# Optimization experiments

Hardware: AMD Instinct MI355X
Metric: run time of the kernel (lower is better)

Reference implementation:

```python
import jax, jax.numpy as jnp
import numpy as np

L = 8          # n_layer
D = 512        # hidden_size
DIN = 1024     # d_inner = 2*D (Mamba expand=2)
DS = 16        # d_state
DTR = 32       # dt_rank = ceil(D/16)
K = 4          # d_conv
NACT = 3       # n_action_to_predict
ADIM = 4
LOSS_COEF = 1.0

def silu(x):
    return x * jax.nn.sigmoid(x)

def rms(x, w, eps=1e-5):
    return x * jax.lax.rsqrt(jnp.mean(x * x, axis=-1, keepdims=True) + eps) * w

def tokenize(images, states, actions, patch_w, patch_b, state_w, state_b, act_w, act_b):
    # images [b,l,3,224,224] -> 14x14 patches of 3*16*16=768 -> mean-pooled image token
    b, l = images.shape[:2]
    p = images.reshape(b, l, 3, 14, 16, 14, 16).transpose(0, 1, 3, 5, 2, 4, 6).reshape(b, l, 196, 768)
    img = jnp.mean(p @ patch_w.T + patch_b, axis=2)            # [b,l,D] token_type 1
    st = states[:, :, 0] @ state_w.T + state_b                 # [b,l,D] token_type 2
    ac = actions[:, :, :NACT - 1] @ act_w.T + act_b            # [b,l,NACT-1,D] token_type 3
    toks = jnp.concatenate([img[:, :, None], st[:, :, None], ac], axis=2)  # [b,l,1+NACT,D]
    return toks.reshape(b, l * (1 + NACT), D)

def mamba_mixer(x, in_w, cw, cb, xpw, dtw, dtb, alog, dp, ow):
    # x: [b,S,D]
    b, S, _ = x.shape
    xz = x @ in_w.T                                   # [b,S,2*DIN]
    xi, z = xz[..., :DIN], xz[..., DIN:]
    # causal depthwise conv, kernel K
    xp = jnp.pad(xi, ((0, 0), (K - 1, 0), (0, 0)))
    xc = cb + sum(cw[:, k] * xp[:, k:k + S, :] for k in range(K))
    xc = silu(xc)
    proj = xc @ xpw.T                                  # [b,S,DTR+2*DS]
    dtr, Bm, Cm = proj[..., :DTR], proj[..., DTR:DTR + DS], proj[..., DTR + DS:]
    dt = jax.nn.softplus(dtr @ dtw.T + dtb)            # [b,S,DIN]
    A = -jnp.exp(alog)                                 # [DIN,DS]
    dA = jnp.exp(dt[..., None] * A)                    # [b,S,DIN,DS]
    dBx = dt[..., None] * Bm[:, :, None, :] * xc[..., None]
    def step(h, inp):
        a_t, bx_t = inp
        h = a_t * h + bx_t
        return h, h
    _, hs = jax.lax.scan(step, jnp.zeros((b, DIN, DS), x.dtype),
                         (dA.swapaxes(0, 1), dBx.swapaxes(0, 1)))  # hs [S,b,DIN,DS]
    y = jnp.einsum('sbdn,bsn->bsd', hs, Cm) + dp * xc
    return (y * silu(z)) @ ow.T

def _forward(images, seq_length, states, actions, action_labels,
             patch_w, patch_b, state_w, state_b, act_w, act_b,
             norm1_w, in_proj_w, conv_w, conv_b, x_proj_w, dt_w, dt_b,
             A_log, Dp, out_proj_w, norm2_w, fc1_w, fc2_w, norm_f_w,
             head_w, head_b):
    b, l = images.shape[:2]
    hidden = tokenize(images, states, actions, patch_w, patch_b, state_w, state_b, act_w, act_b)
    residual = jnp.zeros_like(hidden)
    for i in range(L):
        residual = hidden + residual
        hidden = mamba_mixer(rms(residual, norm1_w[i]), in_proj_w[i], conv_w[i], conv_b[i],
                             x_proj_w[i], dt_w[i], dt_b[i], A_log[i], Dp[i], out_proj_w[i])
        residual = hidden + residual
        g = rms(residual, norm2_w[i]) @ fc1_w[i].T       # GatedMLP fc1 -> [.., 2*DIN]
        hidden = (g[..., :DIN] * silu(g[..., DIN:])) @ fc2_w[i].T
    residual = hidden + residual
    hidden = rms(residual, norm_f_w)
    # static action-token positions: per-frame tokens [img, state, act, act] -> indices 1..3
    hs = hidden.reshape(b, l, 1 + NACT, D)[:, :, 1:, :]
    action_preds = hs @ head_w.T + head_b                # [b,l,NACT,ADIM]
    mask = (jnp.arange(l)[None, :] < seq_length[:, None]).astype(jnp.float32)
    la = jnp.mean(jnp.abs(action_preds - action_labels), axis=(2, 3))
    la = (la * mask).sum(axis=1) / jnp.clip(mask.sum(axis=1), 1.0)
    loss = jnp.mean(la) * LOSS_COEF
    return loss, action_preds

def setup_inputs() -> dict:
    key = jax.random.key(0)
    ks = iter(jax.random.split(key, 40))
    nrm = lambda shape, s=0.02: s * jax.random.normal(next(ks), shape, dtype=jnp.float32)
    inp = {
        'images': jax.random.normal(next(ks), (2, 64, 3, 224, 224), jnp.float32),
        'seq_length': jax.random.randint(next(ks), (2,), 1, 65),
        'states': jax.random.normal(next(ks), (2, 64, NACT, 7), jnp.float32),
        'actions': jax.random.normal(next(ks), (2, 64, NACT, ADIM), jnp.float32),
        'action_labels': jax.random.normal(next(ks), (2, 64, NACT, ADIM), jnp.float32),
        'patch_w': nrm((D, 768)), 'patch_b': jnp.zeros((D,), jnp.float32),
        'state_w': nrm((D, 7)), 'state_b': jnp.zeros((D,), jnp.float32),
        'act_w': nrm((D, ADIM)), 'act_b': jnp.zeros((D,), jnp.float32),
        'norm1_w': jnp.ones((L, D), jnp.float32),
        'in_proj_w': nrm((L, 2 * DIN, D)),
        'conv_w': nrm((L, DIN, K), 0.1), 'conv_b': jnp.zeros((L, DIN), jnp.float32),
        'x_proj_w': nrm((L, DTR + 2 * DS, DIN)),
        'dt_w': nrm((L, DIN, DTR)), 'dt_b': jnp.full((L, DIN), -4.6, jnp.float32),
        'A_log': jnp.log(jnp.broadcast_to(jnp.arange(1, DS + 1, dtype=jnp.float32), (L, DIN, DS))).copy(),
        'Dp': jnp.ones((L, DIN), jnp.float32),
        'out_proj_w': nrm((L, D, DIN)),
        'norm2_w': jnp.ones((L, D), jnp.float32),
        'fc1_w': nrm((L, 2 * DIN, D)), 'fc2_w': nrm((L, D, DIN)),
        'norm_f_w': jnp.ones((D,), jnp.float32),
        'head_w': nrm((ADIM, D)), 'head_b': jnp.zeros((ADIM,), jnp.float32),
    }
    return inp

def reference(images, seq_length, states, actions, action_labels,
              patch_w, patch_b, state_w, state_b, act_w, act_b,
              norm1_w, in_proj_w, conv_w, conv_b, x_proj_w, dt_w, dt_b,
              A_log, Dp, out_proj_w, norm2_w, fc1_w, fc2_w, norm_f_w,
              head_w, head_b):
    return _forward(images, seq_length, states, actions, action_labels,
                    patch_w, patch_b, state_w, state_b, act_w, act_b,
                    norm1_w, in_proj_w, conv_w, conv_b, x_proj_w, dt_w, dt_b,
                    A_log, Dp, out_proj_w, norm2_w, fc1_w, fc2_w, norm_f_w,
                    head_w, head_b)
```

## Files before the change

kernel.cpp:

```cpp
#include <hip/hip_runtime.h>


#define NTOK 512
#define SEQ  256
#define CS   32
#define NC   8

typedef __attribute__((ext_vector_type(8))) short bf16x8;
typedef __attribute__((ext_vector_type(16))) float f32x16;

__device__ __forceinline__ float silu_f(float x) { return x / (1.0f + expf(-x)); }
__device__ __forceinline__ float softplus_f(float x) {
  return (x > 20.0f) ? x : log1pf(expf(x));
}

__device__ __forceinline__ void split_pack(float4 v, uint2* hi, uint2* lo) {
  uint ux = __float_as_uint(v.x), uy = __float_as_uint(v.y);
  uint uz = __float_as_uint(v.z), uw = __float_as_uint(v.w);
  hi->x = (ux >> 16) | (uy & 0xffff0000u);
  hi->y = (uz >> 16) | (uw & 0xffff0000u);
  float lx = v.x - __uint_as_float(ux & 0xffff0000u);
  float ly = v.y - __uint_as_float(uy & 0xffff0000u);
  float lz = v.z - __uint_as_float(uz & 0xffff0000u);
  float lw = v.w - __uint_as_float(uw & 0xffff0000u);
  lo->x = (__float_as_uint(lx) >> 16) | (__float_as_uint(ly) & 0xffff0000u);
  lo->y = (__float_as_uint(lz) >> 16) | (__float_as_uint(lw) & 0xffff0000u);
}

__global__ __launch_bounds__(256) void gemm_bs_k(const float* __restrict__ A,
                                                 const float* __restrict__ B,
                                                 float* __restrict__ C,
                                                 int M, int N, int K, int Kc) {
  __shared__ alignas(16) ushort sAh[2][2][2][512];
  __shared__ alignas(16) ushort sAl[2][2][2][512];
  __shared__ alignas(16) ushort sBh[2][2][2][512];
  __shared__ alignas(16) ushort sBl[2][2][2][512];
  int t = threadIdx.x;
  int bn = blockIdx.x, bm = blockIdx.y, z = blockIdx.z;
  const float* Ab = A + (size_t)bm * 64 * K + (size_t)z * Kc;
  const float* Bb = B + (size_t)bn * 64 * K + (size_t)z * Kc;
  float* Cb = C + (size_t)z * M * N;
  int r = t >> 2, kc = (t & 3) << 2;
  int st = r >> 5, m = r & 31;
  int off = ((kc >> 3) << 8) + (m << 3) + (kc & 7);
  int w = t >> 6, lane = t & 63;
  int wr = w >> 1, wc = w & 1;

  f32x16 acc;
#pragma unroll
  for (int i = 0; i < 16; ++i) acc[i] = 0.f;

  int ns = Kc >> 5;
  const float* Ar = Ab + (size_t)r * K + kc;
  const float* Br = Bb + (size_t)r * K + kc;
  float4 a0 = *(const float4*)&Ar[0];
  float4 a1 = *(const float4*)&Ar[16];
  float4 b0 = *(const float4*)&Br[0];
  float4 b1 = *(const float4*)&Br[16];
  {
    uint2 hi, lo;
    split_pack(a0, &hi, &lo);
    *(uint2*)&sAh[0][0][st][off] = hi; *(uint2*)&sAl[0][0][st][off] = lo;
    split_pack(a1, &hi, &lo);
    *(uint2*)&sAh[0][1][st][off] = hi; *(uint2*)&sAl[0][1][st][off] = lo;
    split_pack(b0, &hi, &lo);
    *(uint2*)&sBh[0][0][st][off] = hi; *(uint2*)&sBl[0][0][st][off] = lo;
    split_pack(b1, &hi, &lo);
    *(uint2*)&sBh[0][1][st][off] = hi; *(uint2*)&sBl[0][1][st][off] = lo;
  }
  __syncthreads();
  for (int ssi = 0; ssi < ns; ++ssi) {
    int buf = ssi & 1;
    if (ssi + 1 < ns) {
      a0 = *(const float4*)&Ar[(ssi + 1) * 32];
      a1 = *(const float4*)&Ar[(ssi + 1) * 32 + 16];
      b0 = *(const float4*)&Br[(ssi + 1) * 32];
      b1 = *(const float4*)&Br[(ssi + 1) * 32 + 16];
    }
    bf16x8 ah = *(bf16x8*)&sAh[buf][0][wr][lane << 3];
    bf16x8 al = *(bf16x8*)&sAl[buf][0][wr][lane << 3];
    bf16x8 bh = *(bf16x8*)&sBh[buf][0][wc][lane << 3];
    bf16x8 bl = *(bf16x8*)&sBl[buf][0][wc][lane << 3];
    acc = __builtin_amdgcn_mfma_f32_32x32x16_bf16(ah, bh, acc, 0, 0, 0);
    acc = __builtin_amdgcn_mfma_f32_32x32x16_bf16(al, bh, acc, 0, 0, 0);
    acc = __builtin_amdgcn_mfma_f32_32x32x16_bf16(ah, bl, acc, 0, 0, 0);
    bf16x8 ah1 = *(bf16x8*)&sAh[buf][1][wr][lane << 3];
    bf16x8 al1 = *(bf16x8*)&sAl[buf][1][wr][lane << 3];
    bf16x8 bh1 = *(bf16x8*)&sBh[buf][1][wc][lane << 3];
    bf16x8 bl1 = *(bf16x8*)&sBl[buf][1][wc][lane << 3];
    acc = __builtin_amdgcn_mfma_f32_32x32x16_bf16(ah1, bh1, acc, 0, 0, 0);
    acc = __builtin_amdgcn_mfma_f32_32x32x16_bf16(al1, bh1, acc, 0, 0, 0);
    acc = __builtin_amdgcn_mfma_f32_32x32x16_bf16(ah1, bl1, acc, 0, 0, 0);
    if (ssi + 1 < ns) {
      uint2 hi, lo;
      split_pack(a0, &hi, &lo);
      *(uint2*)&sAh[buf ^ 1][0][st][off] = hi; *(uint2*)&sAl[buf ^ 1][0][st][off] = lo;
      split_pack(a1, &hi, &lo);
      *(uint2*)&sAh[buf ^ 1][1][st][off] = hi; *(uint2*)&sAl[buf ^ 1][1][st][off] = lo;
      split_pack(b0, &hi, &lo);
      *(uint2*)&sBh[buf ^ 1][0][st][off] = hi; *(uint2*)&sBl[buf ^ 1][0][st][off] = lo;
      split_pack(b1, &hi, &lo);
      *(uint2*)&sBh[buf ^ 1][1][st][off] = hi; *(uint2*)&sBl[buf ^ 1][1][st][off] = lo;
    }
    __syncthreads();
  }
  int col = lane & 31, rq = lane >> 5;
  float* Cw = Cb + (size_t)(bm * 64 + wr * 32) * N + bn * 64 + wc * 32 + col;
#pragma unroll
  for (int rg = 0; rg < 16; ++rg) {
    int row = (rg & 3) + ((rg >> 2) << 3) + (rq << 2);
    Cw[(size_t)row * N] = acc[rg];
  }
}

__global__ __launch_bounds__(256) void gemm_glu_k(const float* __restrict__ G,
                                                  const float* __restrict__ B,
                                                  float* __restrict__ C,
                                                  int M, int N, int K, int Kc) {
  __shared__ alignas(16) ushort sAh[2][2][2][512];
  __shared__ alignas(16) ushort sAl[2][2][2][512];
  __shared__ alignas(16) ushort sBh[2][2][2][512];
  __shared__ alignas(16) ushort sBl[2][2][2][512];
  int t = threadIdx.x;
  int bn = blockIdx.x, bm = blockIdx.y, z = blockIdx.z;
  const float* Gb = G + (size_t)bm * 64 * 2048 + (size_t)z * Kc;
  const float* Bb = B + (size_t)bn * 64 * K + (size_t)z * Kc;
  float* Cb = C + (size_t)z * M * N;
  int r = t >> 2, kc = (t & 3) << 2;
  int st = r >> 5, m = r & 31;
  int off = ((kc >> 3) << 8) + (m << 3) + (kc & 7);
  int w = t >> 6, lane = t & 63;
  int wr = w >> 1, wc = w & 1;

  f32x16 acc;
#pragma unroll
  for (int i = 0; i < 16; ++i) acc[i] = 0.f;

  int ns = Kc >> 5;
  const float* gr = Gb + (size_t)r * 2048 + kc;
  const float* Br = Bb + (size_t)r * K + kc;
  float4 ga0 = *(const float4*)&gr[0];
  float4 gz0 = *(const float4*)&gr[1024];
  float4 ga1 = *(const float4*)&gr[16];
  float4 gz1 = *(const float4*)&gr[1040];
  float4 b0 = *(const float4*)&Br[0];
  float4 b1 = *(const float4*)&Br[16];
  {
    float4 a0 = {ga0.x * silu_f(gz0.x), ga0.y * silu_f(gz0.y),
                 ga0.z * silu_f(gz0.z), ga0.w * silu_f(gz0.w)};
    float4 a1 = {ga1.x * silu_f(gz1.x), ga1.y * silu_f(gz1.y),
                 ga1.z * silu_f(gz1.z), ga1.w * silu_f(gz1.w)};
    uint2 hi, lo;
    split_pack(a0, &hi, &lo);
    *(uint2*)&sAh[0][0][st][off] = hi; *(uint2*)&sAl[0][0][st][off] = lo;
    split_pack(a1, &hi, &lo);
    *(uint2*)&sAh[0][1][st][off] = hi; *(uint2*)&sAl[0][1][st][off] = lo;
    split_pack(b0, &hi, &lo);
    *(uint2*)&sBh[0][0][st][off] = hi; *(uint2*)&sBl[0][0][st][off] = lo;
    split_pack(b1, &hi, &lo);
    *(uint2*)&sBh[0][1][st][off] = hi; *(uint2*)&sBl[0][1][st][off] = lo;
  }
  __syncthreads();
  for (int ssi = 0; ssi < ns; ++ssi) {
    int buf = ssi & 1;
    if (ssi + 1 < ns) {
      ga0 = *(const float4*)&gr[(ssi + 1) * 32];
      gz0 = *(const float4*)&gr[1024 + (ssi + 1) * 32];
      ga1 = *(const float4*)&gr[(ssi + 1) * 32 + 16];
      gz1 = *(const float4*)&gr[1040 + (ssi + 1) * 32];
      b0 = *(const float4*)&Br[(ssi + 1) * 32];
      b1 = *(const float4*)&Br[(ssi + 1) * 32 + 16];
    }
    bf16x8 ah = *(bf16x8*)&sAh[buf][0][wr][lane << 3];
    bf16x8 al = *(bf16x8*)&sAl[buf][0][wr][lane << 3];
    bf16x8 bh = *(bf16x8*)&sBh[buf][0][wc][lane << 3];
    bf16x8 bl = *(bf16x8*)&sBl[buf][0][wc][lane << 3];
    acc = __builtin_amdgcn_mfma_f32_32x32x16_bf16(ah, bh, acc, 0, 0, 0);
    acc = __builtin_amdgcn_mfma_f32_32x32x16_bf16(al, bh, acc, 0, 0, 0);
    acc = __builtin_amdgcn_mfma_f32_32x32x16_bf16(ah, bl, acc, 0, 0, 0);
    bf16x8 ah1 = *(bf16x8*)&sAh[buf][1][wr][lane << 3];
    bf16x8 al1 = *(bf16x8*)&sAl[buf][1][wr][lane << 3];
    bf16x8 bh1 = *(bf16x8*)&sBh[buf][1][wc][lane << 3];
    bf16x8 bl1 = *(bf16x8*)&sBl[buf][1][wc][lane << 3];
    acc = __builtin_amdgcn_mfma_f32_32x32x16_bf16(ah1, bh1, acc, 0, 0, 0);
    acc = __builtin_amdgcn_mfma_f32_32x32x16_bf16(al1, bh1, acc, 0, 0, 0);
    acc = __builtin_amdgcn_mfma_f32_32x32x16_bf16(ah1, bl1, acc, 0, 0, 0);
    if (ssi + 1 < ns) {
      float4 a0 = {ga0.x * silu_f(gz0.x), ga0.y * silu_f(gz0.y),
                   ga0.z * silu_f(gz0.z), ga0.w * silu_f(gz0.w)};
      float4 a1 = {ga1.x * silu_f(gz1.x), ga1.y * silu_f(gz1.y),
                   ga1.z * silu_f(gz1.z), ga1.w * silu_f(gz1.w)};
      uint2 hi, lo;
      split_pack(a0, &hi, &lo);
      *(uint2*)&sAh[buf ^ 1][0][st][off] = hi; *(uint2*)&sAl[buf ^ 1][0][st][off] = lo;
      split_pack(a1, &hi, &lo);
      *(uint2*)&sAh[buf ^ 1][1][st][off] = hi; *(uint2*)&sAl[buf ^ 1][1][st][off] = lo;
      split_pack(b0, &hi, &lo);
      *(uint2*)&sBh[buf ^ 1][0][st][off] = hi; *(uint2*)&sBl[buf ^ 1][0][st][off] = lo;
      split_pack(b1, &hi, &lo);
      *(uint2*)&sBh[buf ^ 1][1][st][off] = hi; *(uint2*)&sBl[buf ^ 1][1][st][off] = lo;
    }
    __syncthreads();
  }
  int col = lane & 31, rq = lane >> 5;
  float* Cw = Cb + (size_t)(bm * 64 + wr * 32) * N + bn * 64 + wc * 32 + col;
#pragma unroll
  for (int rg = 0; rg < 16; ++rg) {
    int row = (rg & 3) + ((rg >> 2) << 3) + (rq << 2);
    Cw[(size_t)row * N] = acc[rg];
  }
}

__global__ void patch_part_k(const float* __restrict__ img, float* __restrict__ pmp) {
  int blk = blockIdx.x;
  int bl = blk / 14, hb = blk % 14;
  int t = threadIdx.x;
  int c = t >> 6, hi = (t >> 2) & 15, wi4 = t & 3;
  const float* base = img + (size_t)bl * 3 * 50176 + (size_t)c * 50176 +
                      (size_t)(hb * 16 + hi) * 224 + wi4 * 4;
  float4 s = {0.f, 0.f, 0.f, 0.f};
#pragma unroll
  for (int wb = 0; wb < 14; ++wb) {
    float4 v = *(const float4*)&base[wb * 16];
    s.x += v.x; s.y += v.y; s.z += v.z; s.w += v.w;
  }
  ((float4*)(pmp + (size_t)blk * 768))[t] = s;
}

__global__ void patch_red_k(const float* __restrict__ pmp, float* __restrict__ meanp) {
  int bl = blockIdx.x;
  int t = threadIdx.x;
  float4 s = {0.f, 0.f, 0.f, 0.f};
  for (int hb = 0; hb < 14; ++hb) {
    float4 v = ((const float4*)(pmp + (size_t)(bl * 14 + hb) * 768))[t];
    s.x += v.x; s.y += v.y; s.z += v.z; s.w += v.w;
  }
  const float inv = 1.0f / 196.0f;
  float4 o = {s.x * inv, s.y * inv, s.z * inv, s.w * inv};
  ((float4*)(meanp + (size_t)bl * 768))[t] = o;
}

__global__ void tokenize_k(const float* __restrict__ imgp,
                           const float* __restrict__ states,
                           const float* __restrict__ actions,
                           const float* __restrict__ pb,
                           const float* __restrict__ sw, const float* __restrict__ sb,
                           const float* __restrict__ aw, const float* __restrict__ ab,
                           float* __restrict__ hidden, float* __restrict__ residual) {
  int tok = blockIdx.x;
  int t = threadIdx.x;
  int j = tok & 3;
  int bl = tok >> 2;
  int o0 = t * 4;
  float out[4];
  if (j == 0) {
    float4 a = ((const float4*)pb)[t];
    const float* ip = imgp + (size_t)bl * 512;
#pragma unroll
    for (int p = 0; p < 8; ++p) {
      float4 v = ((const float4*)(ip + (size_t)p * 65536))[t];
      a.x += v.x; a.y += v.y; a.z += v.z; a.w += v.w;
    }
    out[0] = a.x; out[1] = a.y; out[2] = a.z; out[3] = a.w;
  } else if (j == 1) {
    const float* sv = states + (size_t)bl * 21;
#pragma unroll
    for (int i = 0; i < 4; ++i) {
      int o = o0 + i;
      float acc = sb[o];
      for (int k = 0; k < 7; ++k) acc += sw[o * 7 + k] * sv[k];
      out[i] = acc;
    }
  } else {
    const float* av = actions + ((size_t)bl * 3 + (j - 2)) * 4;
#pragma unroll
    for (int i = 0; i < 4; ++i) {
      int o = o0 + i;
      float acc = ab[o];
      for (int k = 0; k < 4; ++k) acc += aw[o * 4 + k] * av[k];
      out[i] = acc;
    }
  }
  float4 ov = {out[0], out[1], out[2], out[3]};
  ((float4*)(hidden + (size_t)tok * 512))[t] = ov;
  float4 z4 = {0.f, 0.f, 0.f, 0.f};
  ((float4*)(residual + (size_t)tok * 512))[t] = z4;
}

__global__ void addnorm_k(const float* __restrict__ hid, int parts,
                          float* __restrict__ res,
                          const float* __restrict__ w, float* __restrict__ xn) {
  int tok = blockIdx.x;
  int t = threadIdx.x;
  float4* r4 = (float4*)(res + (size_t)tok * 512);
  float4 r = r4[t];
  const float4* hp = (const float4*)(hid + (size_t)tok * 512);
  for (int p = 0; p < parts; ++p) {
    float4 h = hp[t];
    r.x += h.x; r.y += h.y; r.z += h.z; r.w += h.w;
    hp += 65536;
  }
  r4[t] = r;
  float ss = r.x * r.x + r.y * r.y + r.z * r.z + r.w * r.w;
  for (int off = 32; off; off >>= 1) ss += __shfl_down(ss, off, 64);
  __shared__ float s2[2];
  if ((t & 63) == 0) s2[t >> 6] = ss;
  __syncthreads();
  float tot = s2[0] + s2[1];
  float scale = rsqrtf(tot * (1.0f / 512.0f) + 1e-5f);
  float4 wv = ((const float4*)w)[t];
  float4 o = {r.x * scale * wv.x, r.y * scale * wv.y,
              r.z * scale * wv.z, r.w * scale * wv.w};
  ((float4*)(xn + (size_t)tok * 512))[t] = o;
}

__global__ __launch_bounds__(256) void convproj_k(const float* __restrict__ xz,
                                                  const float* __restrict__ cw,
                                                  const float* __restrict__ cb,
                                                  const float* __restrict__ xpw,
                                                  const float* __restrict__ dtw,
                                                  const float* __restrict__ dtbias,
                                                  float* __restrict__ xc,
                                                  float* __restrict__ proj,
                                                  float* __restrict__ dt) {
  int tok = blockIdx.x;
  int t = threadIdx.x;
  int b = tok >> 8, s = tok & 255;
  __shared__ float xr[1024];
  __shared__ float pp[4][64];
  __shared__ float pr[64];
  int d4 = t * 4;
  float4 cw0 = ((const float4*)cw)[d4];
  float4 cw1 = ((const float4*)cw)[d4 + 1];
  float4 cw2 = ((const float4*)cw)[d4 + 2];
  float4 cw3 = ((const float4*)cw)[d4 + 3];
  float acc0 = cb[d4], acc1 = cb[d4 + 1], acc2 = cb[d4 + 2], acc3 = cb[d4 + 3];
  const float* base = xz + (size_t)b * 256 * 2048 + d4;
  const float wk0[4] = {cw0.x, cw0.y, cw0.z, cw0.w};
  const float wk1[4] = {cw1.x, cw1.y, cw1.z, cw1.w};
  const float wk2[4] = {cw2.x, cw2.y, cw2.z, cw2.w};
  const float wk3[4] = {cw3.x, cw3.y, cw3.z, cw3.w};
#pragma unroll
  for (int k = 0; k < 4; ++k) {
    int row = s + k - 3;
    if (row >= 0) {
      float4 v = *(const float4*)&base[(size_t)row * 2048];
      acc0 += wk0[k] * v.x; acc1 += wk1[k] * v.y;
      acc2 += wk2[k] * v.z; acc3 += wk3[k] * v.w;
    }
  }
  float4 xc4 = {silu_f(acc0), silu_f(acc1), silu_f(acc2), silu_f(acc3)};
  ((float4*)(xc + (size_t)tok * 1024))[t] = xc4;
  *(float4*)&xr[d4] = xc4;
  __syncthreads();
  int n = t & 63, q = t >> 6;
  {
    const float* wrow = xpw + (size_t)n * 1024 + q * 256;
    const float* xq = xr + q * 256;
    float acc = 0.f;
    for (int k = 0; k < 256; k += 4)
      acc += wrow[k] * xq[k] + wrow[k + 1] * xq[k + 1] +
             wrow[k + 2] * xq[k + 2] + wrow[k + 3] * xq[k + 3];
    pp[q][n] = acc;
  }
  __syncthreads();
  if (t < 64) {
    float v = pp[0][t] + pp[1][t] + pp[2][t] + pp[3][t];
    pr[t] = v;
    proj[(size_t)tok * 64 + t] = v;
  }
  __syncthreads();
#pragma unroll
  for (int i = 0; i < 4; ++i) {
    int d = t * 4 + i;
    const float* dw = dtw + (size_t)d * 32;
    float a = dtbias[d];
    for (int k = 0; k < 32; ++k) a += dw[k] * pr[k];
    dt[(size_t)tok * 1024 + d] = softplus_f(a);
  }
}

__global__ __launch_bounds__(512) void scan_k(const float* __restrict__ dt,
                                              const float* __restrict__ proj,
                                              const float* __restrict__ xc,
                                              const float* __restrict__ xz,
                                              const float* __restrict__ alog,
                                              const float* __restrict__ Dp,
                                              float* __restrict__ yz) {
  __shared__ float sDt[256][4];
  __shared__ float sXc[256][4];
  __shared__ float sZ[256][4];
  __shared__ float sBC[256][32];
  __shared__ float2 sP[8][4][16];
  __shared__ float sY[256][4];
  int t = threadIdx.x;
  int g = blockIdx.x;
  int b = g >> 8;
  int d0 = (g & 255) << 2;
  int c = t >> 6, dl = (t >> 4) & 3, n = t & 15;
  int d = d0 + dl;
  const float* dtb = dt + (size_t)b * 256 * 1024 + d0;
  const float* xcb = xc + (size_t)b * 256 * 1024 + d0;
  const float* zb  = xz + (size_t)b * 256 * 2048 + 1024 + d0;
  const float* pbp = proj + (size_t)b * 256 * 64 + 32;
  float* yb = yz + (size_t)b * 256 * 1024 + d0;

  if (t < 256) {
    *(float4*)&sDt[t][0] = *(const float4*)&dtb[(size_t)t * 1024];
    *(float4*)&sZ[t][0]  = *(const float4*)&zb[(size_t)t * 2048];
  } else {
    int u = t - 256;
    *(float4*)&sXc[u][0] = *(const float4*)&xcb[(size_t)u * 1024];
  }
#pragma unroll
  for (int i = 0; i < 4; ++i) {
    int idx = i * 512 + t;
    int s = idx >> 3, c4 = (idx & 7) << 2;
    *(float4*)&sBC[s][c4] = *(const float4*)&pbp[(size_t)s * 64 + c4];
  }
  float A = -expf(alog[d * 16 + n]);
  float dp = Dp[d];
  __syncthreads();

  float Ap = 1.f, Bacc = 0.f;
#pragma unroll
  for (int i = 0; i < CS; ++i) {
    int s = (c << 5) + i;
    float dtv = sDt[s][dl];
    float dA = __expf(dtv * A);
    Bacc = dA * Bacc + dtv * sBC[s][n] * sXc[s][dl];
    Ap *= dA;
  }
  sP[c][dl][n] = make_float2(Ap, Bacc);
  __syncthreads();

  float h = 0.f;
  for (int cc = 0; cc < c; ++cc) {
    float2 p = sP[cc][dl][n];
    h = p.x * h + p.y;
  }

#pragma unroll
  for (int i = 0; i < CS; ++i) {
    int s = (c << 5) + i;
    float dtv = sDt[s][dl];
    float xcv = sXc[s][dl];
    float dA = __expf(dtv * A);
    h = dA * h + dtv * sBC[s][n] * xcv;
    float yc = h * sBC[s][16 + n];
    yc += __shfl_xor(yc, 1, 64);
    yc += __shfl_xor(yc, 2, 64);
    yc += __shfl_xor(yc, 4, 64);
    yc += __shfl_xor(yc, 8, 64);
    if (n == 0) sY[s][dl] = (yc + dp * xcv) * silu_f(sZ[s][dl]);
  }
  __syncthreads();
  if (t < 256)
    *(float4*)&yb[(size_t)t * 1024] = *(const float4*)&sY[t][0];
}

__global__ void head_k(const float* __restrict__ hf, const float* __restrict__ hw,
                       const float* __restrict__ hb, const float* __restrict__ labels,
                       float* __restrict__ preds, float* __restrict__ labs) {
  int blk = blockIdx.x;
  int j = blk % 3;
  int l = (blk / 3) % 64;
  int b = blk / 192;
  int row = b * 256 + l * 4 + 1 + j;
  int t = threadIdx.x;
  const float* x = hf + (size_t)row * 512;
  float acc[4] = {0.f, 0.f, 0.f, 0.f};
  for (int k = t; k < 512; k += 64) {
    float xv = x[k];
#pragma unroll
    for (int a = 0; a < 4; ++a) acc[a] += xv * hw[a * 512 + k];
  }
  for (int off = 32; off; off >>= 1) {
#pragma unroll
    for (int a = 0; a < 4; ++a) acc[a] += __shfl_down(acc[a], off, 64);
  }
  if (t == 0) {
    const float* lab = labels + (size_t)blk * 4;
    float sd = 0.f;
#pragma unroll
    for (int a = 0; a < 4; ++a) {
      float p = acc[a] + hb[a];
      preds[(size_t)blk * 4 + a] = p;
      sd += fabsf(p - lab[a]);
    }
    labs[blk] = sd;
  }
}

__global__ void loss_k(const float* __restrict__ labs, const int* __restrict__ seqlen,
                       float* __restrict__ out) {
  int t = threadIdx.x;
  int b = t >> 6, l = t & 63;
  float la = (labs[(b * 64 + l) * 3] + labs[(b * 64 + l) * 3 + 1] +
              labs[(b * 64 + l) * 3 + 2]) * (1.0f / 12.0f);
  float m = (l < seqlen[b]) ? 1.f : 0.f;
  float v = la * m;
  for (int off = 32; off; off >>= 1) {
    v += __shfl_down(v, off, 64);
    m += __shfl_down(m, off, 64);
  }
  __shared__ float sb_[2];
  if ((t & 63) == 0) sb_[b] = v / fmaxf(m, 1.0f);
  __syncthreads();
  if (t == 0) out[0] = 0.5f * (sb_[0] + sb_[1]);
}

extern "C" void kernel_launch(void* const* d_in, const int* in_sizes, int n_in,
                              void* d_out, int out_size, void* d_ws, size_t ws_size,
                              hipStream_t stream) {
  const float* images     = (const float*)d_in[0];
  const int*   seq_length = (const int*)d_in[1];
  const float* states     = (const float*)d_in[2];
  const float* actions    = (const float*)d_in[3];
  const float* labels     = (const float*)d_in[4];
  const float* patch_w    = (const float*)d_in[5];
  const float* patch_b    = (const float*)d_in[6];
  const float* state_w    = (const float*)d_in[7];
  const float* state_b    = (const float*)d_in[8];
  const float* act_w      = (const float*)d_in[9];
  const float* act_b      = (const float*)d_in[10];
  const float* norm1_w    = (const float*)d_in[11];
  const float* in_proj_w  = (const float*)d_in[12];
  const float* conv_w     = (const float*)d_in[13];
  const float* conv_b     = (const float*)d_in[14];
  const float* x_proj_w   = (const float*)d_in[15];
  const float* dt_w       = (const float*)d_in[16];
  const float* dt_b       = (const float*)d_in[17];
  const float* A_log      = (const float*)d_in[18];
  const float* Dp         = (const float*)d_in[19];
  const float* out_proj_w = (const float*)d_in[20];
  const float* norm2_w    = (const float*)d_in[21];
  const float* fc1_w      = (const float*)d_in[22];
  const float* fc2_w      = (const float*)d_in[23];
  const float* norm_f_w   = (const float*)d_in[24];
  const float* head_w     = (const float*)d_in[25];
  const float* head_b     = (const float*)d_in[26];

  float* out = (float*)d_out;

  float* ws = (float*)d_ws;
  float* meanp    = ws; ws += 98304;
  float* hidden   = ws; ws += 262144;
  float* residual = ws; ws += 262144;
  float* xn       = ws; ws += 262144;
  float* xz       = ws; ws += 1048576;
  float* xc       = ws; ws += 524288;
  float* proj     = ws; ws += 32768;
  float* dtbuf    = ws; ws += 524288;
  float* yz       = ws; ws += 524288;
  float* labs     = ws; ws += 384;
  float* cpart    = ws; ws += 1048576;
  float* pmp      = ws; ws += 1376256;

  hipLaunchKernelGGL(patch_part_k, dim3(1792), dim3(192), 0, stream, images, pmp);
  hipLaunchKernelGGL(patch_red_k, dim3(128), dim3(192), 0, stream, pmp, meanp);
  hipLaunchKernelGGL(gemm_bs_k, dim3(8, 2, 8), dim3(256), 0, stream,
                     meanp, patch_w, cpart, 128, 512, 768, 96);
  hipLaunchKernelGGL(tokenize_k, dim3(512), dim3(128), 0, stream, cpart, states, actions,
                     patch_b, state_w, state_b, act_w, act_b, hidden, residual);

  for (int i = 0; i < 8; ++i) {
    const float* n1 = norm1_w + i * 512;
    const float* ipw = in_proj_w + (size_t)i * 2048 * 512;
    const float* cw = conv_w + (size_t)i * 4096;
    const float* cb = conv_b + (size_t)i * 1024;
    const float* xpw = x_proj_w + (size_t)i * 65536;
    const float* dtw = dt_w + (size_t)i * 32768;
    const float* dtbias = dt_b + (size_t)i * 1024;
    const float* al = A_log + (size_t)i * 16384;
    const float* dpp = Dp + (size_t)i * 1024;
    const float* opw = out_proj_w + (size_t)i * 524288;
    const float* n2 = norm2_w + i * 512;
    const float* f1 = fc1_w + (size_t)i * 1048576;
    const float* f2 = fc2_w + (size_t)i * 524288;

    if (i == 0)
      hipLaunchKernelGGL(addnorm_k, dim3(512), dim3(128), 0, stream,
                         hidden, 1, residual, n1, xn);
    else
      hipLaunchKernelGGL(addnorm_k, dim3(512), dim3(128), 0, stream,
                         cpart, 4, residual, n1, xn);
    hipLaunchKernelGGL(gemm_bs_k, dim3(32, 8, 1), dim3(256), 0, stream,
                       xn, ipw, xz, 512, 2048, 512, 512);
    hipLaunchKernelGGL(convproj_k, dim3(512), dim3(256), 0, stream,
                       xz, cw, cb, xpw, dtw, dtbias, xc, proj, dtbuf);
    hipLaunchKernelGGL(scan_k, dim3(512), dim3(512), 0, stream,
                       dtbuf, proj, xc, xz, al, dpp, yz);
    hipLaunchKernelGGL(gemm_bs_k, dim3(8, 8, 4), dim3(256), 0, stream,
                       yz, opw, cpart, 512, 512, 1024, 256);
    hipLaunchKernelGGL(addnorm_k, dim3(512), dim3(128), 0, stream,
                       cpart, 4, residual, n2, xn);
    hipLaunchKernelGGL(gemm_bs_k, dim3(32, 8, 1), dim3(256), 0, stream,
                       xn, f1, xz, 512, 2048, 512, 512);
    hipLaunchKernelGGL(gemm_glu_k, dim3(8, 8, 4), dim3(256), 0, stream,
                       xz, f2, cpart, 512, 512, 1024, 256);
  }

  hipLaunchKernelGGL(addnorm_k, dim3(512), dim3(128), 0, stream,
                     cpart, 4, residual, norm_f_w, xn);
  hipLaunchKernelGGL(head_k, dim3(384), dim3(64), 0, stream, xn, head_w, head_b, labels,
                     out + 1, labs);
  hipLaunchKernelGGL(loss_k, dim3(1), dim3(128), 0, stream, labs, seq_length, out);
}
```

Before: 1.117 ms.

## Fuse per-layer kernels into one persistent cooperative megakernel with grid syncs

Replaces the roughly 70 separate kernel launches (GEMMs, addnorm, conv/proj, scan, tokenize, head, loss) with a single cooperative persistent kernel. Each stage loops over virtual blocks and is separated from the next by grid.sync(), with shared memory overlaid through a union-like buffer. The aim is to remove launch overhead and inter-kernel gaps. In exchange, the grid is capped by occupancy, so stages may serialize over fewer blocks, and every grid barrier has its own cost. Addnorm is adapted to 256 threads with float2.

```diff
diff --git a/kernel.cpp b/kernel.cpp
--- a/kernel.cpp
+++ b/kernel.cpp
@@ -1,10 +1,8 @@
 #include <hip/hip_runtime.h>
-
-
-#define NTOK 512
-#define SEQ  256
-#define CS   32
-#define NC   8
+#include <hip/hip_cooperative_groups.h>
+
+namespace cg = cooperative_groups;
+
 
 typedef __attribute__((ext_vector_type(8))) short bf16x8;
 typedef __attribute__((ext_vector_type(16))) float f32x16;
@@ -27,16 +25,33 @@
   lo->y = (__float_as_uint(lz) >> 16) | (__float_as_uint(lw) & 0xffff0000u);
 }
 
-__global__ __launch_bounds__(256) void gemm_bs_k(const float* __restrict__ A,
-                                                 const float* __restrict__ B,
-                                                 float* __restrict__ C,
-                                                 int M, int N, int K, int Kc) {
-  __shared__ alignas(16) ushort sAh[2][2][2][512];
-  __shared__ alignas(16) ushort sAl[2][2][2][512];
-  __shared__ alignas(16) ushort sBh[2][2][2][512];
-  __shared__ alignas(16) ushort sBl[2][2][2][512];
-  int t = threadIdx.x;
-  int bn = blockIdx.x, bm = blockIdx.y, z = blockIdx.z;
+struct GemmLds {
+  ushort sAh[2][2][2][512];
+  ushort sAl[2][2][2][512];
+  ushort sBh[2][2][2][512];
+  ushort sBl[2][2][2][512];
+};
+struct ScanLds {
+  float sDt[256][4];
+  float sXc[256][4];
+  float sZ[256][4];
+  float sBC[256][32];
+  float2 sP[8][4][16];
+  float sY[256][4];
+};
+struct ConvLds {
+  float xr[1024];
+  float pp[4][64];
+  float pr[64];
+};
+#define SMEM_BYTES 53248
+
+__device__ __forceinline__ void st_gemm(const float* __restrict__ A,
+                                        const float* __restrict__ B,
+                                        float* __restrict__ C,
+                                        int M, int N, int K, int Kc,
+                                        int bn, int bm, int z, int t, char* smem) {
+  GemmLds& L = *(GemmLds*)smem;
   const float* Ab = A + (size_t)bm * 64 * K + (size_t)z * Kc;
   const float* Bb = B + (size_t)bn * 64 * K + (size_t)z * Kc;
   float* Cb = C + (size_t)z * M * N;
@@ -60,13 +75,13 @@
   {
     uint2 hi, lo;
     split_pack(a0, &hi, &lo);
-    *(uint2*)&sAh[0][0][st][off] = hi; *(uint2*)&sAl[0][0][st][off] = lo;
+    *(uint2*)&L.sAh[0][0][st][off] = hi; *(uint2*)&L.sAl[0][0][st][off] = lo;
     split_pack(a1, &hi, &lo);
-    *(uint2*)&sAh[0][1][st][off] = hi; *(uint2*)&sAl[0][1][st][off] = lo;
+    *(uint2*)&L.sAh[0][1][st][off] = hi; *(uint2*)&L.sAl[0][1][st][off] = lo;
     split_pack(b0, &hi, &lo);
-    *(uint2*)&sBh[0][0][st][off] = hi; *(uint2*)&sBl[0][0][st][off] = lo;
+    *(uint2*)&L.sBh[0][0][st][off] = hi; *(uint2*)&L.sBl[0][0][st][off] = lo;
     split_pack(b1, &hi, &lo);
-    *(uint2*)&sBh[0][1][st][off] = hi; *(uint2*)&sBl[0][1][st][off] = lo;
+    *(uint2*)&L.sBh[0][1][st][off] = hi; *(uint2*)&L.sBl[0][1][st][off] = lo;
   }
   __syncthreads();
   for (int ssi = 0; ssi < ns; ++ssi) {
@@ -77,30 +92,30 @@
       b0 = *(const float4*)&Br[(ssi + 1) * 32];
       b1 = *(const float4*)&Br[(ssi + 1) * 32 + 16];
     }
-    bf16x8 ah = *(bf16x8*)&sAh[buf][0][wr][lane << 3];
-    bf16x8 al = *(bf16x8*)&sAl[buf][0][wr][lane << 3];
-    bf16x8 bh = *(bf16x8*)&sBh[buf][0][wc][lane << 3];
-    bf16x8 bl = *(bf16x8*)&sBl[buf][0][wc][lane << 3];
+    bf16x8 ah = *(bf16x8*)&L.sAh[buf][0][wr][lane << 3];
+    bf16x8 al = *(bf16x8*)&L.sAl[buf][0][wr][lane << 3];
+    bf16x8 bh = *(bf16x8*)&L.sBh[buf][0][wc][lane << 3];
+    bf16x8 bl = *(bf16x8*)&L.sBl[buf][0][wc][lane << 3];
     acc = __builtin_amdgcn_mfma_f32_32x32x16_bf16(ah, bh, acc, 0, 0, 0);
     acc = __builtin_amdgcn_mfma_f32_32x32x16_bf16(al, bh, acc, 0, 0, 0);
     acc = __builtin_amdgcn_mfma_f32_32x32x16_bf16(ah, bl, acc, 0, 0, 0);
-    bf16x8 ah1 = *(bf16x8*)&sAh[buf][1][wr][lane << 3];
-    bf16x8 al1 = *(bf16x8*)&sAl[buf][1][wr][lane << 3];
-    bf16x8 bh1 = *(bf16x8*)&sBh[buf][1][wc][lane << 3];
-    bf16x8 bl1 = *(bf16x8*)&sBl[buf][1][wc][lane << 3];
+    bf16x8 ah1 = *(bf16x8*)&L.sAh[buf][1][wr][lane << 3];
+    bf16x8 al1 = *(bf16x8*)&L.sAl[buf][1][wr][lane << 3];
+    bf16x8 bh1 = *(bf16x8*)&L.sBh[buf][1][wc][lane << 3];
+    bf16x8 bl1 = *(bf16x8*)&L.sBl[buf][1][wc][lane << 3];
     acc = __builtin_amdgcn_mfma_f32_32x32x16_bf16(ah1, bh1, acc, 0, 0, 0);
     acc = __builtin_amdgcn_mfma_f32_32x32x16_bf16(al1, bh1, acc, 0, 0, 0);
     acc = __builtin_amdgcn_mfma_f32_32x32x16_bf16(ah1, bl1, acc, 0, 0, 0);
     if (ssi + 1 < ns) {
       uint2 hi, lo;
       split_pack(a0, &hi, &lo);
-      *(uint2*)&sAh[buf ^ 1][0][st][off] = hi; *(uint2*)&sAl[buf ^ 1][0][st][off] = lo;
+      *(uint2*)&L.sAh[buf ^ 1][0][st][off] = hi; *(uint2*)&L.sAl[buf ^ 1][0][st][off] = lo;
       split_pack(a1, &hi, &lo);
-      *(uint2*)&sAh[buf ^ 1][1][st][off] = hi; *(uint2*)&sAl[buf ^ 1][1][st][off] = lo;
+      *(uint2*)&L.sAh[buf ^ 1][1][st][off] = hi; *(uint2*)&L.sAl[buf ^ 1][1][st][off] = lo;
       split_pack(b0, &hi, &lo);
-      *(uint2*)&sBh[buf ^ 1][0][st][off] = hi; *(uint2*)&sBl[buf ^ 1][0][st][off] = lo;
+      *(uint2*)&L.sBh[buf ^ 1][0][st][off] = hi; *(uint2*)&L.sBl[buf ^ 1][0][st][off] = lo;
       split_pack(b1, &hi, &lo);
-      *(uint2*)&sBh[buf ^ 1][1][st][off] = hi; *(uint2*)&sBl[buf ^ 1][1][st][off] = lo;
+      *(uint2*)&L.sBh[buf ^ 1][1][st][off] = hi; *(uint2*)&L.sBl[buf ^ 1][1][st][off] = lo;
     }
     __syncthreads();
   }
@@ -113,16 +128,12 @@
   }
 }
 
-__global__ __launch_bounds__(256) void gemm_glu_k(const float* __restrict__ G,
-                                                  const float* __restrict__ B,
-                                                  float* __restrict__ C,
-                                                  int M, int N, int K, int Kc) {
-  __shared__ alignas(16) ushort sAh[2][2][2][512];
-  __shared__ alignas(16) ushort sAl[2][2][2][512];
-  __shared__ alignas(16) ushort sBh[2][2][2][512];
-  __shared__ alignas(16) ushort sBl[2][2][2][512];
-  int t = threadIdx.x;
-  int bn = blockIdx.x, bm = blockIdx.y, z = blockIdx.z;
+__device__ __forceinline__ void st_glu(const float* __restrict__ G,
+                                       const float* __restrict__ B,
+                                       float* __restrict__ C,
+                                       int M, int N, int K, int Kc,
+                                       int bn, int bm, int z, int t, char* smem) {
+  GemmLds& L = *(GemmLds*)smem;
   const float* Gb = G + (size_t)bm * 64 * 2048 + (size_t)z * Kc;
   const float* Bb = B + (size_t)bn * 64 * K + (size_t)z * Kc;
   float* Cb = C + (size_t)z * M * N;
@@ -152,13 +163,13 @@
                  ga1.z * silu_f(gz1.z), ga1.w * silu_f(gz1.w)};
     uint2 hi, lo;
     split_pack(a0, &hi, &lo);
-    *(uint2*)&sAh[0][0][st][off] = hi; *(uint2*)&sAl[0][0][st][off] = lo;
+    *(uint2*)&L.sAh[0][0][st][off] = hi; *(uint2*)&L.sAl[0][0][st][off] = lo;
     split_pack(a1, &hi, &lo);
-    *(uint2*)&sAh[0][1][st][off] = hi; *(uint2*)&sAl[0][1][st][off] = lo;
+    *(uint2*)&L.sAh[0][1][st][off] = hi; *(uint2*)&L.sAl[0][1][st][off] = lo;
     split_pack(b0, &hi, &lo);
-    *(uint2*)&sBh[0][0][st][off] = hi; *(uint2*)&sBl[0][0][st][off] = lo;
+    *(uint2*)&L.sBh[0][0][st][off] = hi; *(uint2*)&L.sBl[0][0][st][off] = lo;
     split_pack(b1, &hi, &lo);
-    *(uint2*)&sBh[0][1][st][off] = hi; *(uint2*)&sBl[0][1][st][off] = lo;
+    *(uint2*)&L.sBh[0][1][st][off] = hi; *(uint2*)&L.sBl[0][1][st][off] = lo;
   }
   __syncthreads();
   for (int ssi = 0; ssi < ns; ++ssi) {
@@ -171,17 +182,17 @@
       b0 = *(const float4*)&Br[(ssi + 1) * 32];
       b1 = *(const float4*)&Br[(ssi + 1) * 32 + 16];
     }
-    bf16x8 ah = *(bf16x8*)&sAh[buf][0][wr][lane << 3];
-    bf16x8 al = *(bf16x8*)&sAl[buf][0][wr][lane << 3];
-    bf16x8 bh = *(bf16x8*)&sBh[buf][0][wc][lane << 3];
-    bf16x8 bl = *(bf16x8*)&sBl[buf][0][wc][lane << 3];
+    bf16x8 ah = *(bf16x8*)&L.sAh[buf][0][wr][lane << 3];
+    bf16x8 al = *(bf16x8*)&L.sAl[buf][0][wr][lane << 3];
+    bf16x8 bh = *(bf16x8*)&L.sBh[buf][0][wc][lane << 3];
+    bf16x8 bl = *(bf16x8*)&L.sBl[buf][0][wc][lane << 3];
     acc = __builtin_amdgcn_mfma_f32_32x32x16_bf16(ah, bh, acc, 0, 0, 0);
     acc = __builtin_amdgcn_mfma_f32_32x32x16_bf16(al, bh, acc, 0, 0, 0);
     acc = __builtin_amdgcn_mfma_f32_32x32x16_bf16(ah, bl, acc, 0, 0, 0);
-    bf16x8 ah1 = *(bf16x8*)&sAh[buf][1][wr][lane << 3];
-    bf16x8 al1 = *(bf16x8*)&sAl[buf][1][wr][lane << 3];
-    bf16x8 bh1 = *(bf16x8*)&sBh[buf][1][wc][lane << 3];
-    bf16x8 bl1 = *(bf16x8*)&sBl[buf][1][wc][lane << 3];
+    bf16x8 ah1 = *(bf16x8*)&L.sAh[buf][1][wr][lane << 3];
+    bf16x8 al1 = *(bf16x8*)&L.sAl[buf][1][wr][lane << 3];
+    bf16x8 bh1 = *(bf16x8*)&L.sBh[buf][1][wc][lane << 3];
+    bf16x8 bl1 = *(bf16x8*)&L.sBl[buf][1][wc][lane << 3];
     acc = __builtin_amdgcn_mfma_f32_32x32x16_bf16(ah1, bh1, acc, 0, 0, 0);
     acc = __builtin_amdgcn_mfma_f32_32x32x16_bf16(al1, bh1, acc, 0, 0, 0);
     acc = __builtin_amdgcn_mfma_f32_32x32x16_bf16(ah1, bl1, acc, 0, 0, 0);
@@ -192,13 +203,13 @@
                    ga1.z * silu_f(gz1.z), ga1.w * silu_f(gz1.w)};
       uint2 hi, lo;
       split_pack(a0, &hi, &lo);
-      *(uint2*)&sAh[buf ^ 1][0][st][off] = hi; *(uint2*)&sAl[buf ^ 1][0][st][off] = lo;
+      *(uint2*)&L.sAh[buf ^ 1][0][st][off] = hi; *(uint2*)&L.sAl[buf ^ 1][0][st][off] = lo;
       split_pack(a1, &hi, &lo);
-      *(uint2*)&sAh[buf ^ 1][1][st][off] = hi; *(uint2*)&sAl[buf ^ 1][1][st][off] = lo;
+      *(uint2*)&L.sAh[buf ^ 1][1][st][off] = hi; *(uint2*)&L.sAl[buf ^ 1][1][st][off] = lo;
       split_pack(b0, &hi, &lo);
-      *(uint2*)&sBh[buf ^ 1][0][st][off] = hi; *(uint2*)&sBl[buf ^ 1][0][st][off] = lo;
+      *(uint2*)&L.sBh[buf ^ 1][0][st][off] = hi; *(uint2*)&L.sBl[buf ^ 1][0][st][off] = lo;
       split_pack(b1, &hi, &lo);
-      *(uint2*)&sBh[buf ^ 1][1][st][off] = hi; *(uint2*)&sBl[buf ^ 1][1][st][off] = lo;
+      *(uint2*)&L.sBh[buf ^ 1][1][st][off] = hi; *(uint2*)&L.sBl[buf ^ 1][1][st][off] = lo;
     }
     __syncthreads();
   }
@@ -211,44 +222,18 @@
   }
 }
 
-__global__ void patch_part_k(const float* __restrict__ img, float* __restrict__ pmp) {
-  int blk = blockIdx.x;
-  int bl = blk / 14, hb = blk % 14;
-  int t = threadIdx.x;
-  int c = t >> 6, hi = (t >> 2) & 15, wi4 = t & 3;
-  const float* base = img + (size_t)bl * 3 * 50176 + (size_t)c * 50176 +
-                      (size_t)(hb * 16 + hi) * 224 + wi4 * 4;
-  float4 s = {0.f, 0.f, 0.f, 0.f};
-#pragma unroll
-  for (int wb = 0; wb < 14; ++wb) {
-    float4 v = *(const float4*)&base[wb * 16];
-    s.x += v.x; s.y += v.y; s.z += v.z; s.w += v.w;
-  }
-  ((float4*)(pmp + (size_t)blk * 768))[t] = s;
-}
-
-__global__ void patch_red_k(const float* __restrict__ pmp, float* __restrict__ meanp) {
-  int bl = blockIdx.x;
-  int t = threadIdx.x;
-  float4 s = {0.f, 0.f, 0.f, 0.f};
-  for (int hb = 0; hb < 14; ++hb) {
-    float4 v = ((const float4*)(pmp + (size_t)(bl * 14 + hb) * 768))[t];
-    s.x += v.x; s.y += v.y; s.z += v.z; s.w += v.w;
-  }
-  const float inv = 1.0f / 196.0f;
-  float4 o = {s.x * inv, s.y * inv, s.z * inv, s.w * inv};
-  ((float4*)(meanp + (size_t)bl * 768))[t] = o;
-}
-
-__global__ void tokenize_k(const float* __restrict__ imgp,
-                           const float* __restrict__ states,
-                           const float* __restrict__ actions,
-                           const float* __restrict__ pb,
-                           const float* __restrict__ sw, const float* __restrict__ sb,
-                           const float* __restrict__ aw, const float* __restrict__ ab,
-                           float* __restrict__ hidden, float* __restrict__ residual) {
-  int tok = blockIdx.x;
-  int t = threadIdx.x;
+__device__ __forceinline__ void st_tokenize(const float* __restrict__ imgp,
+                                            const float* __restrict__ states,
+                                            const float* __restrict__ actions,
+                                            const float* __restrict__ pb,
+                                            const float* __restrict__ sw,
+                                            const float* __restrict__ sb,
+                                            const float* __restrict__ aw,
+                                            const float* __restrict__ ab,
+                                            float* __restrict__ hidden,
+                                            float* __restrict__ residual,
+                                            int tok, int t) {
+  if (t >= 128) return;
   int j = tok & 3;
   int bl = tok >> 2;
   int o0 = t * 4;
@@ -287,48 +272,45 @@
   ((float4*)(residual + (size_t)tok * 512))[t] = z4;
 }
 
-__global__ void addnorm_k(const float* __restrict__ hid, int parts,
-                          float* __restrict__ res,
-                          const float* __restrict__ w, float* __restrict__ xn) {
-  int tok = blockIdx.x;
-  int t = threadIdx.x;
-  float4* r4 = (float4*)(res + (size_t)tok * 512);
-  float4 r = r4[t];
-  const float4* hp = (const float4*)(hid + (size_t)tok * 512);
+__device__ __forceinline__ void st_addnorm(const float* __restrict__ hid, int parts,
+                                           float* __restrict__ res,
+                                           const float* __restrict__ w,
+                                           float* __restrict__ xn,
+                                           int tok, int t, char* smem) {
+  float* s2 = (float*)smem;
+  float2* r2 = (float2*)(res + (size_t)tok * 512);
+  float2 r = r2[t];
+  const float2* hp = (const float2*)(hid + (size_t)tok * 512);
   for (int p = 0; p < parts; ++p) {
-    float4 h = hp[t];
-    r.x += h.x; r.y += h.y; r.z += h.z; r.w += h.w;
-    hp += 65536;
-  }
-  r4[t] = r;
-  float ss = r.x * r.x + r.y * r.y + r.z * r.z + r.w * r.w;
+    float2 h = hp[t];
+    r.x += h.x; r.y += h.y;
+    hp += 131072;
+  }
+  r2[t] = r;
+  float ss = r.x * r.x + r.y * r.y;
   for (int off = 32; off; off >>= 1) ss += __shfl_down(ss, off, 64);
-  __shared__ float s2[2];
   if ((t & 63) == 0) s2[t >> 6] = ss;
   __syncthreads();
-  float tot = s2[0] + s2[1];
+  float tot = s2[0] + s2[1] + s2[2] + s2[3];
   float scale = rsqrtf(tot * (1.0f / 512.0f) + 1e-5f);
-  float4 wv = ((const float4*)w)[t];
-  float4 o = {r.x * scale * wv.x, r.y * scale * wv.y,
-              r.z * scale * wv.z, r.w * scale * wv.w};
-  ((float4*)(xn + (size_t)tok * 512))[t] = o;
-}
-
-__global__ __launch_bounds__(256) void convproj_k(const float* __restrict__ xz,
-                                                  const float* __restrict__ cw,
-                                                  const float* __restrict__ cb,
-                                                  const float* __restrict__ xpw,
-                                                  const float* __restrict__ dtw,
-                                                  const float* __restrict__ dtbias,
-                                                  float* __restrict__ xc,
-                                                  float* __restrict__ proj,
-                                                  float* __restrict__ dt) {
-  int tok = blockIdx.x;
-  int t = threadIdx.x;
+  float2 wv = ((const float2*)w)[t];
+  float2 o = {r.x * scale * wv.x, r.y * scale * wv.y};
+  ((float2*)(xn + (size_t)tok * 512))[t] = o;
+  __syncthreads();
+}
+
+__device__ __forceinline__ void st_conv(const float* __restrict__ xz,
+                                        const float* __restrict__ cw,
+                                        const float* __restrict__ cb,
+                                        const float* __restrict__ xpw,
+                                        const float* __restrict__ dtw,
+                                        const float* __restrict__ dtbias,
+                                        float* __restrict__ xc,
+                                        float* __restrict__ proj,
+                                        float* __restrict__ dt,
+                                        int tok, int t, char* smem) {
+  ConvLds& L = *(ConvLds*)smem;
   int b = tok >> 8, s = tok & 255;
-  __shared__ float xr[1024];
-  __shared__ float pp[4][64];
-  __shared__ float pr[64];
   int d4 = t * 4;
   float4 cw0 = ((const float4*)cw)[d4];
   float4 cw1 = ((const float4*)cw)[d4 + 1];
@@ -351,22 +333,22 @@
   }
   float4 xc4 = {silu_f(acc0), silu_f(acc1), silu_f(acc2), silu_f(acc3)};
   ((float4*)(xc + (size_t)tok * 1024))[t] = xc4;
-  *(float4*)&xr[d4] = xc4;
+  *(float4*)&L.xr[d4] = xc4;
   __syncthreads();
   int n = t & 63, q = t >> 6;
   {
     const float* wrow = xpw + (size_t)n * 1024 + q * 256;
-    const float* xq = xr + q * 256;
+    const float* xq = L.xr + q * 256;
     float acc = 0.f;
     for (int k = 0; k < 256; k += 4)
       acc += wrow[k] * xq[k] + wrow[k + 1] * xq[k + 1] +
              wrow[k + 2] * xq[k + 2] + wrow[k + 3] * xq[k + 3];
-    pp[q][n] = acc;
+    L.pp[q][n] = acc;
   }
   __syncthreads();
   if (t < 64) {
-    float v = pp[0][t] + pp[1][t] + pp[2][t] + pp[3][t];
-    pr[t] = v;
+    float v = L.pp[0][t] + L.pp[1][t] + L.pp[2][t] + L.pp[3][t];
+    L.pr[t] = v;
     proj[(size_t)tok * 64 + t] = v;
   }
   __syncthreads();
@@ -375,29 +357,23 @@
     int d = t * 4 + i;
     const float* dw = dtw + (size_t)d * 32;
     float a = dtbias[d];
-    for (int k = 0; k < 32; ++k) a += dw[k] * pr[k];
+    for (int k = 0; k < 32; ++k) a += dw[k] * L.pr[k];
     dt[(size_t)tok * 1024 + d] = softplus_f(a);
   }
 }
 
-__global__ __launch_bounds__(512) void scan_k(const float* __restrict__ dt,
-                                              const float* __restrict__ proj,
-                                              const float* __restrict__ xc,
-                                              const float* __restrict__ xz,
-                                              const float* __restrict__ alog,
-                                              const float* __restrict__ Dp,
-                                              float* __restrict__ yz) {
-  __shared__ float sDt[256][4];
-  __shared__ float sXc[256][4];
-  __shared__ float sZ[256][4];
-  __shared__ float sBC[256][32];
-  __shared__ float2 sP[8][4][16];
-  __shared__ float sY[256][4];
-  int t = threadIdx.x;
-  int g = blockIdx.x;
-  int b = g >> 8;
-  int d0 = (g & 255) << 2;
-  int c = t >> 6, dl = (t >> 4) & 3, n = t & 15;
+__device__ __forceinline__ void st_scan(const float* __restrict__ dt,
+                                        const float* __restrict__ proj,
+                                        const float* __restrict__ xc,
+                                        const float* __restrict__ xz,
+                                        const float* __restrict__ alog,
+                                        const float* __restrict__ Dp,
+                                        float* __restrict__ yz,
+                                        int vb, int t, char* smem) {
+  ScanLds& L = *(ScanLds*)smem;
+  int b = vb >> 8;
+  int d0 = (vb & 255) << 2;
+  int c2 = t >> 6, dl = (t >> 4) & 3, n = t & 15;
   int d = d0 + dl;
   const float* dtb = dt + (size_t)b * 256 * 1024 + d0;
   const float* xcb = xc + (size_t)b * 256 * 1024 + d0;
@@ -405,69 +381,81 @@
   const float* pbp = proj + (size_t)b * 256 * 64 + 32;
   float* yb = yz + (size_t)b * 256 * 1024 + d0;
 
-  if (t < 256) {
-    *(float4*)&sDt[t][0] = *(const float4*)&dtb[(size_t)t * 1024];
-    *(float4*)&sZ[t][0]  = *(const float4*)&zb[(size_t)t * 2048];
-  } else {
-    int u = t - 256;
-    *(float4*)&sXc[u][0] = *(const float4*)&xcb[(size_t)u * 1024];
-  }
-#pragma unroll
-  for (int i = 0; i < 4; ++i) {
-    int idx = i * 512 + t;
+  *(float4*)&L.sDt[t][0] = *(const float4*)&dtb[(size_t)t * 1024];
+  *(float4*)&L.sXc[t][0] = *(const float4*)&xcb[(size_t)t * 1024];
+  *(float4*)&L.sZ[t][0]  = *(const float4*)&zb[(size_t)t * 2048];
+#pragma unroll
+  for (int i = 0; i < 8; ++i) {
+    int idx = i * 256 + t;
     int s = idx >> 3, c4 = (idx & 7) << 2;
-    *(float4*)&sBC[s][c4] = *(const float4*)&pbp[(size_t)s * 64 + c4];
+    *(float4*)&L.sBC[s][c4] = *(const float4*)&pbp[(size_t)s * 64 + c4];
   }
   float A = -expf(alog[d * 16 + n]);
   float dp = Dp[d];
   __syncthreads();
 
-  float Ap = 1.f, Bacc = 0.f;
-#pragma unroll
-  for (int i = 0; i < CS; ++i) {
-    int s = (c << 5) + i;
-    float dtv = sDt[s][dl];
-    float dA = __expf(dtv * A);
-    Bacc = dA * Bacc + dtv * sBC[s][n] * sXc[s][dl];
-    Ap *= dA;
-  }
-  sP[c][dl][n] = make_float2(Ap, Bacc);
+#pragma unroll
+  for (int half = 0; half < 2; ++half) {
+    int c = c2 + half * 4;
+    float Ap = 1.f, Bacc = 0.f;
+#pragma unroll
+    for (int i = 0; i < 32; ++i) {
+      int s = (c << 5) + i;
+      float dtv = L.sDt[s][dl];
+      float dA = __expf(dtv * A);
+      Bacc = dA * Bacc + dtv * L.sBC[s][n] * L.sXc[s][dl];
+      Ap *= dA;
+    }
+    L.sP[c][dl][n] = make_float2(Ap, Bacc);
+  }
   __syncthreads();
 
   float h = 0.f;
-  for (int cc = 0; cc < c; ++cc) {
-    float2 p = sP[cc][dl][n];
+  for (int cc = 0; cc < c2; ++cc) {
+    float2 p = L.sP[cc][dl][n];
     h = p.x * h + p.y;
   }
-
-#pragma unroll
-  for (int i = 0; i < CS; ++i) {
-    int s = (c << 5) + i;
-    float dtv = sDt[s][dl];
-    float xcv = sXc[s][dl];
-    float dA = __expf(dtv * A);
-    h = dA * h + dtv * sBC[s][n] * xcv;
-    float yc = h * sBC[s][16 + n];
-    yc += __shfl_xor(yc, 1, 64);
-    yc += __shfl_xor(yc, 2, 64);
-    yc += __shfl_xor(yc, 4, 64);
-    yc += __shfl_xor(yc, 8, 64);
-    if (n == 0) sY[s][dl] = (yc + dp * xcv) * silu_f(sZ[s][dl]);
-  }
-  __syncthreads();
-  if (t < 256)
-    *(float4*)&yb[(size_t)t * 1024] = *(const float4*)&sY[t][0];
-}
-
-__global__ void head_k(const float* __restrict__ hf, const float* __restrict__ hw,
-                       const float* __restrict__ hb, const float* __restrict__ labels,
-                       float* __restrict__ preds, float* __restrict__ labs) {
-  int blk = blockIdx.x;
+#pragma unroll
+  for (int half = 0; half < 2; ++half) {
+    int c = c2 + half * 4;
+    if (half) {
+      for (int cc = c2 + 1; cc < c2 + 4; ++cc) {
+        float2 p = L.sP[cc][dl][n];
+        h = p.x * h + p.y;
+      }
+    }
+#pragma unroll
+    for (int i = 0; i < 32; ++i) {
+      int s = (c << 5) + i;
+      float dtv = L.sDt[s][dl];
+      float xcv = L.sXc[s][dl];
+      float dA = __expf(dtv * A);
+      h = dA * h + dtv * L.sBC[s][n] * xcv;
+      float yc = h * L.sBC[s][16 + n];
+      yc += __shfl_xor(yc, 1, 64);
+      yc += __shfl_xor(yc, 2, 64);
+      yc += __shfl_xor(yc, 4, 64);
+      yc += __shfl_xor(yc, 8, 64);
+      if (n == 0) L.sY[s][dl] = (yc + dp * xcv) * silu_f(L.sZ[s][dl]);
+    }
+  }
+  __syncthreads();
+  *(float4*)&yb[(size_t)t * 1024] = *(const float4*)&L.sY[t][0];
+  __syncthreads();
+}
+
+__device__ __forceinline__ void st_head(const float* __restrict__ hf,
+                                        const float* __restrict__ hw,
+                                        const float* __restrict__ hb,
+                                        const float* __restrict__ labels,
+                                        float* __restrict__ preds,
+                                        float* __restrict__ labs,
+                                        int blk, int t) {
+  if (t >= 64) return;
   int j = blk % 3;
   int l = (blk / 3) % 64;
   int b = blk / 192;
   int row = b * 256 + l * 4 + 1 + j;
-  int t = threadIdx.x;
   const float* x = hf + (size_t)row * 512;
   float acc[4] = {0.f, 0.f, 0.f, 0.f};
   for (int k = t; k < 512; k += 64) {
@@ -492,22 +480,133 @@
   }
 }
 
-__global__ void loss_k(const float* __restrict__ labs, const int* __restrict__ seqlen,
-                       float* __restrict__ out) {
+__device__ __forceinline__ void st_loss(const float* __restrict__ labs,
+                                        const int* __restrict__ seqlen,
+                                        float* __restrict__ out, int t, char* smem) {
+  float* sb_ = (float*)smem;
+  if (t < 128) {
+    int b = t >> 6, l = t & 63;
+    float la = (labs[(b * 64 + l) * 3] + labs[(b * 64 + l) * 3 + 1] +
+                labs[(b * 64 + l) * 3 + 2]) * (1.0f / 12.0f);
+    float m = (l < seqlen[b]) ? 1.f : 0.f;
+    float v = la * m;
+    for (int off = 32; off; off >>= 1) {
+      v += __shfl_down(v, off, 64);
+      m += __shfl_down(m, off, 64);
+    }
+    if ((t & 63) == 0) sb_[b] = v / fmaxf(m, 1.0f);
+  }
+  __syncthreads();
+  if (t == 0) out[0] = 0.5f * (sb_[0] + sb_[1]);
+}
+
+__global__ __launch_bounds__(256, 2) void mega_k(
+    const float* states, const float* actions, const float* patch_b,
+    const float* state_w, const float* state_b, const float* act_w,
+    const float* act_b, const float* patch_w,
+    const float* norm1_w, const float* in_proj_w, const float* conv_w,
+    const float* conv_b, const float* x_proj_w, const float* dt_w,
+    const float* dt_b, const float* A_log, const float* Dp,
+    const float* out_proj_w, const float* norm2_w, const float* fc1_w,
+    const float* fc2_w, const float* norm_f_w, const float* head_w,
+    const float* head_b, const float* labels, const int* seq_length,
+    float* meanp, float* hidden, float* residual, float* xn, float* xz,
+    float* xc, float* proj, float* dtbuf, float* yz, float* labs,
+    float* cpart, float* out) {
+  __shared__ alignas(16) char smem[SMEM_BYTES];
+  cg::grid_group grid = cg::this_grid();
+  int g = blockIdx.x, t = threadIdx.x, nb = gridDim.x;
+
+  for (int vb = g; vb < 128; vb += nb)
+    st_gemm(meanp, patch_w, cpart, 128, 512, 768, 96,
+            vb & 7, (vb >> 3) & 1, vb >> 4, t, smem);
+  grid.sync();
+  for (int vb = g; vb < 512; vb += nb)
+    st_tokenize(cpart, states, actions, patch_b, state_w, state_b,
+                act_w, act_b, hidden, residual, vb, t);
+  grid.sync();
+
+  for (int i = 0; i < 8; ++i) {
+    const float* n1 = norm1_w + i * 512;
+    const float* ipw = in_proj_w + (size_t)i * 2048 * 512;
+    const float* cw = conv_w + (size_t)i * 4096;
+    const float* cb = conv_b + (size_t)i * 1024;
+    const float* xpw = x_proj_w + (size_t)i * 65536;
+    const float* dtw = dt_w + (size_t)i * 32768;
+    const float* dtbias = dt_b + (size_t)i * 1024;
+    const float* al = A_log + (size_t)i * 16384;
+    const float* dpp = Dp + (size_t)i * 1024;
+    const float* opw = out_proj_w + (size_t)i * 524288;
+    const float* n2 = norm2_w + i * 512;
+    const float* f1 = fc1_w + (size_t)i * 1048576;
+    const float* f2 = fc2_w + (size_t)i * 524288;
+    const float* hid_in = (i == 0) ? hidden : cpart;
+    int parts = (i == 0) ? 1 : 4;
+
+    for (int vb = g; vb < 512; vb += nb)
+      st_addnorm(hid_in, parts, residual, n1, xn, vb, t, smem);
+    grid.sync();
+    for (int vb = g; vb < 256; vb += nb)
+      st_gemm(xn, ipw, xz, 512, 2048, 512, 512, vb & 31, vb >> 5, 0, t, smem);
+    grid.sync();
+    for (int vb = g; vb < 512; vb += nb)
+      st_conv(xz, cw, cb, xpw, dtw, dtbias, xc, proj, dtbuf, vb, t, smem);
+    grid.sync();
+    for (int vb = g; vb < 512; vb += nb)
+      st_scan(dtbuf, proj, xc, xz, al, dpp, yz, vb, t, smem);
+    grid.sync();
+    for (int vb = g; vb < 256; vb += nb)
+      st_gemm(yz, opw, cpart, 512, 512, 1024, 256,
+              vb & 7, (vb >> 3) & 7, vb >> 6, t, smem);
+    grid.sync();
+    for (int vb = g; vb < 512; vb += nb)
+      st_addnorm(cpart, 4, residual, n2, xn, vb, t, smem);
+    grid.sync();
+    for (int vb = g; vb < 256; vb += nb)
+      st_gemm(xn, f1, xz, 512, 2048, 512, 512, vb & 31, vb >> 5, 0, t, smem);
+    grid.sync();
+    for (int vb = g; vb < 256; vb += nb)
+      st_glu(xz, f2, cpart, 512, 512, 1024, 256,
+             vb & 7, (vb >> 3) & 7, vb >> 6, t, smem);
+    grid.sync();
+  }
+
+  for (int vb = g; vb < 512; vb += nb)
+    st_addnorm(cpart, 4, residual, norm_f_w, xn, vb, t, smem);
+  grid.sync();
+  for (int vb = g; vb < 384; vb += nb)
+    st_head(xn, head_w, head_b, labels, out + 1, labs, vb, t);
+  grid.sync();
+  if (g == 0) st_loss(labs, seq_length, out, t, smem);
+}
+
+__global__ void patch_part_k(const float* __restrict__ img, float* __restrict__ pmp) {
+  int blk = blockIdx.x;
+  int bl = blk / 14, hb = blk % 14;
   int t = threadIdx.x;
-  int b = t >> 6, l = t & 63;
-  float la = (labs[(b * 64 + l) * 3] + labs[(b * 64 + l) * 3 + 1] +
-              labs[(b * 64 + l) * 3 + 2]) * (1.0f / 12.0f);
-  float m = (l < seqlen[b]) ? 1.f : 0.f;
-  float v = la * m;
-  for (int off = 32; off; off >>= 1) {
-    v += __shfl_down(v, off, 64);
-    m += __shfl_down(m, off, 64);
-  }
-  __shared__ float sb_[2];
-  if ((t & 63) == 0) sb_[b] = v / fmaxf(m, 1.0f);
-  __syncthreads();
-  if (t == 0) out[0] = 0.5f * (sb_[0] + sb_[1]);
+  int c = t >> 6, hi = (t >> 2) & 15, wi4 = t & 3;
+  const float* base = img + (size_t)bl * 3 * 50176 + (size_t)c * 50176 +
+                      (size_t)(hb * 16 + hi) * 224 + wi4 * 4;
+  float4 s = {0.f, 0.f, 0.f, 0.f};
+#pragma unroll
+  for (int wb = 0; wb < 14; ++wb) {
+    float4 v = *(const float4*)&base[wb * 16];
+    s.x += v.x; s.y += v.y; s.z += v.z; s.w += v.w;
+  }
+  ((float4*)(pmp + (size_t)blk * 768))[t] = s;
+}
+
+__global__ void patch_red_k(const float* __restrict__ pmp, float* __restrict__ meanp) {
+  int bl = blockIdx.x;
+  int t = threadIdx.x;
+  float4 s = {0.f, 0.f, 0.f, 0.f};
+  for (int hb = 0; hb < 14; ++hb) {
+    float4 v = ((const float4*)(pmp + (size_t)(bl * 14 + hb) * 768))[t];
+    s.x += v.x; s.y += v.y; s.z += v.z; s.w += v.w;
+  }
+  const float inv = 1.0f / 196.0f;
+  float4 o = {s.x * inv, s.y * inv, s.z * inv, s.w * inv};
+  ((float4*)(meanp + (size_t)bl * 768))[t] = o;
 }
 
 extern "C" void kernel_launch(void* const* d_in, const int* in_sizes, int n_in,
@@ -559,51 +658,33 @@
 
   hipLaunchKernelGGL(patch_part_k, dim3(1792), dim3(192), 0, stream, images, pmp);
   hipLaunchKernelGGL(patch_red_k, dim3(128), dim3(192), 0, stream, pmp, meanp);
-  hipLaunchKernelGGL(gemm_bs_k, dim3(8, 2, 8), dim3(256), 0, stream,
-                     meanp, patch_w, cpart, 128, 512, 768, 96);
-  hipLaunchKernelGGL(tokenize_k, dim3(512), dim3(128), 0, stream, cpart, states, actions,
-                     patch_b, state_w, state_b, act_w, act_b, hidden, residual);
-
-  for (int i = 0; i < 8; ++i) {
-    const float* n1 = norm1_w + i * 512;
-    const float* ipw = in_proj_w + (size_t)i * 2048 * 512;
-    const float* cw = conv_w + (size_t)i * 4096;
-    const float* cb = conv_b + (size_t)i * 1024;
-    const float* xpw = x_proj_w + (size_t)i * 65536;
-    const float* dtw = dt_w + (size_t)i * 32768;
-    const float* dtbias = dt_b + (size_t)i * 1024;
-    const float* al = A_log + (size_t)i * 16384;
-    const float* dpp = Dp + (size_t)i * 1024;
-    const float* opw = out_proj_w + (size_t)i * 524288;
-    const float* n2 = norm2_w + i * 512;
-    const float* f1 = fc1_w + (size_t)i * 1048576;
-    const float* f2 = fc2_w + (size_t)i * 524288;
-
-    if (i == 0)
-      hipLaunchKernelGGL(addnorm_k, dim3(512), dim3(128), 0, stream,
-                         hidden, 1, residual, n1, xn);
-    else
-      hipLaunchKernelGGL(addnorm_k, dim3(512), dim3(128), 0, stream,
-                         cpart, 4, residual, n1, xn);
-    hipLaunchKernelGGL(gemm_bs_k, dim3(32, 8, 1), dim3(256), 0, stream,
-                       xn, ipw, xz, 512, 2048, 512, 512);
-    hipLaunchKernelGGL(convproj_k, dim3(512), dim3(256), 0, stream,
-                       xz, cw, cb, xpw, dtw, dtbias, xc, proj, dtbuf);
-    hipLaunchKernelGGL(scan_k, dim3(512), dim3(512), 0, stream,
-                       dtbuf, proj, xc, xz, al, dpp, yz);
-    hipLaunchKernelGGL(gemm_bs_k, dim3(8, 8, 4), dim3(256), 0, stream,
-                       yz, opw, cpart, 512, 512, 1024, 256);
-    hipLaunchKernelGGL(addnorm_k, dim3(512), dim3(128), 0, stream,
-                       cpart, 4, residual, n2, xn);
-    hipLaunchKernelGGL(gemm_bs_k, dim3(32, 8, 1), dim3(256), 0, stream,
-                       xn, f1, xz, 512, 2048, 512, 512);
-    hipLaunchKernelGGL(gemm_glu_k, dim3(8, 8, 4), dim3(256), 0, stream,
-                       xz, f2, cpart, 512, 512, 1024, 256);
-  }
-
-  hipLaunchKernelGGL(addnorm_k, dim3(512), dim3(128), 0, stream,
-                     cpart, 4, residual, norm_f_w, xn);
-  hipLaunchKernelGGL(head_k, dim3(384), dim3(64), 0, stream, xn, head_w, head_b, labels,
-                     out + 1, labs);
-  hipLaunchKernelGGL(loss_k, dim3(1), dim3(128), 0, stream, labs, seq_length, out);
-}
+
+  static int nblk = 0;
+  if (nblk == 0) {
+    int maxBlk = 0;
+    hipOccupancyMaxActiveBlocksPerMultiprocessor(&maxBlk, mega_k, 256, 0);
+    if (maxBlk < 1) maxBlk = 1;
+    int dev = 0;
+    hipGetDevice(&dev);
+    hipDeviceProp_t prop;
+    hipGetDeviceProperties(&prop, dev);
+    int cap = maxBlk * prop.multiProcessorCount;
+    nblk = cap >= 512 ? 512 : (cap >= 256 ? 256 : cap);
+  }
+
+  void* kargs[] = {
+    (void*)&states, (void*)&actions, (void*)&patch_b,
+    (void*)&state_w, (void*)&state_b, (void*)&act_w, (void*)&act_b,
+    (void*)&patch_w,
+    (void*)&norm1_w, (void*)&in_proj_w, (void*)&conv_w, (void*)&conv_b,
+    (void*)&x_proj_w, (void*)&dt_w, (void*)&dt_b, (void*)&A_log, (void*)&Dp,
+    (void*)&out_proj_w, (void*)&norm2_w, (void*)&fc1_w, (void*)&fc2_w,
+    (void*)&norm_f_w, (void*)&head_w, (void*)&head_b,
+    (void*)&labels, (void*)&seq_length,
+    (void*)&meanp, (void*)&hidden, (void*)&residual, (void*)&xn, (void*)&xz,
+    (void*)&xc, (void*)&proj, (void*)&dtbuf, (void*)&yz, (void*)&labs,
+    (void*)&cpart, (void*)&out
+  };
+  hipLaunchCooperativeKernel((const void*)mega_k, dim3(nblk), dim3(256),
+                             kargs, 0, stream);
+}
```

Measured after the change: 3.458 ms. 210% more time.
